# Performance work log

Measured on AMD Instinct MI355X. Metric: run time of the kernel, lower is better.

Reference implementation:

```python
import jax, jax.numpy as jnp
import numpy as np

CONV_LAYERS = [10, 10, 10]
DILATIONS = [1 << l for nl in CONV_LAYERS for l in range(nl)]  # 30 layers
B, C, S, V = 128, 64, 256, 256


def setup_inputs() -> dict:
    key = jax.random.key(0)
    ks = jax.random.split(key, 12)
    L = len(DILATIONS)
    sc = 0.1  # keep gated activations away from saturation
    return {
        "waveform_seed": jax.random.randint(ks[0], (B,), 0, V, dtype=jnp.int32),
        "embedding": jax.random.normal(ks[1], (V, C), jnp.float32) * sc,
        "kernels": jax.random.normal(ks[2], (L, 2, C, 2 * C), jnp.float32) * sc,
        "conv_bias": jax.random.normal(ks[3], (L, 2 * C), jnp.float32) * sc,
        "res_w": jax.random.normal(ks[4], (L, C, C), jnp.float32) * sc,
        "res_b": jax.random.normal(ks[5], (L, C), jnp.float32) * sc,
        "skip_w": jax.random.normal(ks[6], (L, C, S), jnp.float32) * sc,
        "skip_b": jax.random.normal(ks[7], (L, S), jnp.float32) * sc,
        "out_w0": jax.random.normal(ks[8], (S, V), jnp.float32) * sc,
        "out_b0": jax.random.normal(ks[9], (V,), jnp.float32) * sc,
        "out_w1": jax.random.normal(ks[10], (V, V), jnp.float32) * sc,
        "out_b1": jax.random.normal(ks[11], (V,), jnp.float32) * sc,
        "max_infer_samples": 128,
    }


def wavenet_generate(waveform_seed, embedding, kernels, conv_bias, res_w, res_b,
                     skip_w, skip_b, out_w0, out_b0, out_w1, out_b1, T):
    # Per-layer dilation queues (the tf queue_lst), initialized to zeros.
    bufs0 = tuple(jnp.zeros((d, B, C), embedding.dtype) for d in DILATIONS)

    def step(carry, _):
        bufs, idx = carry
        x = embedding[idx]                                   # (B, C) embedding lookup
        skip = jnp.zeros((B, S), x.dtype)
        new_bufs = []
        for i in range(len(DILATIONS)):
            buf = bufs[i]                                    # (d_i, B, C)
            x_last = buf[0]                                  # queue.pop(0)
            new_bufs.append(jnp.concatenate([buf[1:], x[None]], axis=0))  # queue.append(x_cur)
            # k=2 causal conv == two matmuls on (x_last, x_cur)
            h = x_last @ kernels[i, 0] + x @ kernels[i, 1] + conv_bias[i]  # (B, 2C)
            g = jnp.tanh(h[:, :C]) * jax.nn.sigmoid(h[:, C:])              # gated activation
            x = x + g @ res_w[i] + res_b[i]                   # residual out -> next layer input
            skip = skip + g @ skip_w[i] + skip_b[i]           # skip accumulation
        skip = jax.nn.relu(skip)
        h0 = jax.nn.relu(skip @ out_w0 + out_b0)
        logits = h0 @ out_w1 + out_b1                         # (B, V)
        nxt = jnp.argmax(logits, axis=-1).astype(jnp.int32)   # deterministic sampling
        return (tuple(new_bufs), nxt), (nxt, logits)

    _, (samples, logits) = jax.lax.scan(step, (bufs0, waveform_seed), None, length=T)
    # samples: (T, B) -> (B, T); logits: (T, B, V) -> (B, T, V)
    return samples.T, jnp.transpose(logits, (1, 0, 2))


def reference(waveform_seed, embedding, kernels, conv_bias, res_w, res_b,
              skip_w, skip_b, out_w0, out_b0, out_w1, out_b1, max_infer_samples):
    return wavenet_generate(waveform_seed, embedding, kernels, conv_bias, res_w, res_b,
                            skip_w, skip_b, out_w0, out_b0, out_w1, out_b1,
                            max_infer_samples)
```

## Files before the change

kernel.cpp:

```cpp
#include <hip/hip_runtime.h>
#include <hip/hip_bf16.h>
#include <math.h>


#define NL 30
#define NC 64
#define NS 256
#define NV 256
#define NB 128
#define QTOT 3069

__device__ float g_queues[(size_t)NB * QTOT * NC];

__global__ __launch_bounds__(256, 1)
void wavenet_gen_kernel(const int* __restrict__ seed,
                        const float* __restrict__ emb,
                        const float* __restrict__ kern,
                        const float* __restrict__ cbias,
                        const float* __restrict__ resw,
                        const float* __restrict__ resb,
                        const float* __restrict__ skipw,
                        const float* __restrict__ skipb,
                        const float* __restrict__ w0,
                        const float* __restrict__ b0,
                        const float* __restrict__ w1,
                        const float* __restrict__ b1,
                        const int* __restrict__ pT,
                        float* __restrict__ out)
{
  const int b = blockIdx.x;
  const int tid = threadIdx.x;
  const int T = pT[0];

  __shared__ float sx[NC];
  __shared__ float sxl[NC];
  __shared__ float shp[2][2 * NC];
  __shared__ float sg[NC];
  __shared__ float sskip[NS];
  __shared__ float sh0[NV];
  __shared__ float rv[4];
  __shared__ int   ri[4];
  __shared__ int   snext;

  if (tid < NC) sx[tid] = emb[(size_t)seed[b] * NC + tid];
  __syncthreads();

  float* __restrict__ q = g_queues + (size_t)b * QTOT * NC;
  const size_t logits_base = (size_t)NB * (size_t)T;

  for (int t = 0; t < T; ++t) {
    float skipacc = 0.f;
    int qoff = 0;

    for (int i = 0; i < NL; ++i) {
      const int d = 1 << (i % 10);

      if (tid < NC) {
        const int slot = t & (d - 1);
        float* qs = q + (size_t)(qoff + slot) * NC + tid;
        sxl[tid] = (t >= d) ? *qs : 0.f;
        *qs = sx[tid];
      }
      __syncthreads();

      {
        const int j = tid & 127;
        const int half = tid >> 7;
        const float* __restrict__ W =
            kern + ((size_t)(i * 2 + half)) * NC * 2 * NC + j;
        const float* __restrict__ xv = half ? sx : sxl;
        float acc = 0.f;
#pragma unroll
        for (int c = 0; c < NC; ++c) acc = fmaf(xv[c], W[(size_t)c * 2 * NC], acc);
        shp[half][j] = acc;
      }
      __syncthreads();

      if (tid < NC) {
        const float ha = shp[0][tid] + shp[1][tid] + cbias[i * 2 * NC + tid];
        const float hb = shp[0][tid + NC] + shp[1][tid + NC] + cbias[i * 2 * NC + NC + tid];
        sg[tid] = tanhf(ha) * (1.f / (1.f + expf(-hb)));
      }
      __syncthreads();

      {
        const float* __restrict__ SW = skipw + (size_t)i * NC * NS + tid;
        float acc = 0.f;
#pragma unroll
        for (int c = 0; c < NC; ++c) acc = fmaf(sg[c], SW[(size_t)c * NS], acc);
        skipacc += acc + skipb[i * NS + tid];
      }
      if (tid < NC) {
        const float* __restrict__ RW = resw + (size_t)i * NC * NC + tid;
        float acc = 0.f;
#pragma unroll
        for (int c = 0; c < NC; ++c) acc = fmaf(sg[c], RW[(size_t)c * NC], acc);
        sx[tid] = sx[tid] + acc + resb[i * NC + tid];
      }
      qoff += d;
      __syncthreads();
    }

    sskip[tid] = fmaxf(skipacc, 0.f);
    __syncthreads();
    {
      const float* __restrict__ W = w0 + tid;
      float acc = 0.f;
#pragma unroll 8
      for (int s = 0; s < NS; ++s) acc = fmaf(sskip[s], W[(size_t)s * NV], acc);
      sh0[tid] = fmaxf(acc + b0[tid], 0.f);
    }
    __syncthreads();
    float lg;
    {
      const float* __restrict__ W = w1 + tid;
      float acc = 0.f;
#pragma unroll 8
      for (int s = 0; s < NV; ++s) acc = fmaf(sh0[s], W[(size_t)s * NV], acc);
      lg = acc + b1[tid];
      out[logits_base + ((size_t)b * T + t) * NV + tid] = lg;
    }

    float v = lg;
    int ix = tid;
#pragma unroll
    for (int o = 32; o > 0; o >>= 1) {
      float ov = __shfl_down(v, o);
      int oi = __shfl_down(ix, o);
      if (ov > v || (ov == v && oi < ix)) { v = ov; ix = oi; }
    }
    if ((tid & 63) == 0) { rv[tid >> 6] = v; ri[tid >> 6] = ix; }
    __syncthreads();
    if (tid == 0) {
      float bv = rv[0];
      int bi = ri[0];
#pragma unroll
      for (int w = 1; w < 4; ++w)
        if (rv[w] > bv || (rv[w] == bv && ri[w] < bi)) { bv = rv[w]; bi = ri[w]; }
      snext = bi;
      out[(size_t)b * T + t] = (float)bi;
    }
    __syncthreads();

    if (tid < NC) sx[tid] = emb[(size_t)snext * NC + tid];
    __syncthreads();
  }
}

extern "C" void kernel_launch(void* const* d_in, const int* in_sizes, int n_in,
                              void* d_out, int out_size, void* d_ws, size_t ws_size,
                              hipStream_t stream) {
  (void)in_sizes; (void)n_in; (void)out_size; (void)d_ws; (void)ws_size;
  wavenet_gen_kernel<<<NB, 256, 0, stream>>>(
      (const int*)d_in[0],   (const float*)d_in[1], (const float*)d_in[2],
      (const float*)d_in[3], (const float*)d_in[4], (const float*)d_in[5],
      (const float*)d_in[6], (const float*)d_in[7], (const float*)d_in[8],
      (const float*)d_in[9], (const float*)d_in[10], (const float*)d_in[11],
      (const int*)d_in[12],  (float*)d_out);
}
```

Before: 14.15 ms.

## Split dot products across 4 threads and move queue traffic out of layer loop

Raises the block from 256 to 1024 threads, and splits every dot product over 4 lanes that are combined with xor shuffles, so each layer's serial FMA chain becomes a quarter as long. Per-layer queue reads and writes are taken off the critical path. Each layer's input is kept in a shared history buffer, and all 30 layers' delayed inputs are prefetched for the next step after the layer loop. This also removes one barrier per layer by merging the residual and skip phases. The cost is more threads per block, extra shuffle reductions and more shared memory.

```diff
diff --git a/kernel.cpp b/kernel.cpp
--- a/kernel.cpp
+++ b/kernel.cpp
@@ -9,10 +9,18 @@
 #define NV 256
 #define NB 128
 #define QTOT 3069
+#define NT 1024
 
 __device__ float g_queues[(size_t)NB * QTOT * NC];
 
-__global__ __launch_bounds__(256, 1)
+__device__ __forceinline__ void layer_params(int l, int& d, int& qo) {
+  const int a = (l >= 20) ? 2 : ((l >= 10) ? 1 : 0);
+  const int bb = l - a * 10;
+  d = 1 << bb;
+  qo = a * 1023 + (d - 1);
+}
+
+__global__ __launch_bounds__(NT, 1)
 void wavenet_gen_kernel(const int* __restrict__ seed,
                         const float* __restrict__ emb,
                         const float* __restrict__ kern,
@@ -28,21 +36,30 @@
                         const int* __restrict__ pT,
                         float* __restrict__ out)
 {
-  const int b = blockIdx.x;
-  const int tid = threadIdx.x;
-  const int T = pT[0];
-
-  __shared__ float sx[NC];
-  __shared__ float sxl[NC];
-  __shared__ float shp[2][2 * NC];
+  const int b   = blockIdx.x;
+  const int t_  = threadIdx.x;
+  const int T   = pT[0];
+
+  const int j    = t_ >> 2;
+  const int p    = t_ & 3;
+  const int half = j >> 7;
+  const int col  = j & 127;
+  const int lane = t_ & 63;
+  const int wv   = t_ >> 6;
+
+  __shared__ float sxlAll[NL][NC];
+  __shared__ float xHist[NL][NC];
+  __shared__ float hp[2][2 * NC];
   __shared__ float sg[NC];
   __shared__ float sskip[NS];
   __shared__ float sh0[NV];
-  __shared__ float rv[4];
-  __shared__ int   ri[4];
+  __shared__ float rv[16];
+  __shared__ int   ri[16];
   __shared__ int   snext;
 
-  if (tid < NC) sx[tid] = emb[(size_t)seed[b] * NC + tid];
+  ((float*)sxlAll)[t_] = 0.f;
+  if (t_ < (NL * NC - NT)) ((float*)sxlAll)[t_ + NT] = 0.f;
+  if (t_ < NC) xHist[0][t_] = emb[(size_t)seed[b] * NC + t_];
   __syncthreads();
 
   float* __restrict__ q = g_queues + (size_t)b * QTOT * NC;
@@ -50,99 +67,140 @@
 
   for (int t = 0; t < T; ++t) {
     float skipacc = 0.f;
-    int qoff = 0;
 
     for (int i = 0; i < NL; ++i) {
-      const int d = 1 << (i % 10);
-
-      if (tid < NC) {
-        const int slot = t & (d - 1);
-        float* qs = q + (size_t)(qoff + slot) * NC + tid;
-        sxl[tid] = (t >= d) ? *qs : 0.f;
-        *qs = sx[tid];
+      {
+        const float* __restrict__ W =
+            kern + ((size_t)(i * 2 + half)) * NC * (2 * NC) + col;
+        const float* __restrict__ xv = half ? xHist[i] : sxlAll[i];
+        float acc = 0.f;
+#pragma unroll
+        for (int cc = 0; cc < 16; ++cc) {
+          const int c = p * 16 + cc;
+          acc = fmaf(xv[c], W[(size_t)c * (2 * NC)], acc);
+        }
+        acc += __shfl_xor(acc, 1);
+        acc += __shfl_xor(acc, 2);
+        if (p == 0) hp[half][col] = acc;
       }
       __syncthreads();
 
+      if (t_ < NC) {
+        const float ha = hp[0][t_] + hp[1][t_] + cbias[i * 2 * NC + t_];
+        const float hb = hp[0][NC + t_] + hp[1][NC + t_] + cbias[i * 2 * NC + NC + t_];
+        sg[t_] = tanhf(ha) * (1.f / (1.f + expf(-hb)));
+      }
+      __syncthreads();
+
       {
-        const int j = tid & 127;
-        const int half = tid >> 7;
-        const float* __restrict__ W =
-            kern + ((size_t)(i * 2 + half)) * NC * 2 * NC + j;
-        const float* __restrict__ xv = half ? sx : sxl;
+        const float* __restrict__ SW = skipw + (size_t)i * NC * NS + j;
         float acc = 0.f;
 #pragma unroll
-        for (int c = 0; c < NC; ++c) acc = fmaf(xv[c], W[(size_t)c * 2 * NC], acc);
-        shp[half][j] = acc;
-      }
+        for (int cc = 0; cc < 16; ++cc) {
+          const int c = p * 16 + cc;
+          acc = fmaf(sg[c], SW[(size_t)c * NS], acc);
+        }
+        acc += __shfl_xor(acc, 1);
+        acc += __shfl_xor(acc, 2);
+        skipacc += acc + skipb[i * NS + j];
+      }
+      if (i < NL - 1 && t_ < 256) {
+        const float* __restrict__ RW = resw + (size_t)i * NC * NC + j;
+        float acc = 0.f;
+#pragma unroll
+        for (int cc = 0; cc < 16; ++cc) {
+          const int c = p * 16 + cc;
+          acc = fmaf(sg[c], RW[(size_t)c * NC], acc);
+        }
+        acc += __shfl_xor(acc, 1);
+        acc += __shfl_xor(acc, 2);
+        if (p == 0) xHist[i + 1][j] = xHist[i][j] + acc + resb[i * NC + j];
+      }
+      if (i == NL - 1 && p == 0) sskip[j] = fmaxf(skipacc, 0.f);
       __syncthreads();
-
-      if (tid < NC) {
-        const float ha = shp[0][tid] + shp[1][tid] + cbias[i * 2 * NC + tid];
-        const float hb = shp[0][tid + NC] + shp[1][tid + NC] + cbias[i * 2 * NC + NC + tid];
-        sg[tid] = tanhf(ha) * (1.f / (1.f + expf(-hb)));
-      }
-      __syncthreads();
-
-      {
-        const float* __restrict__ SW = skipw + (size_t)i * NC * NS + tid;
-        float acc = 0.f;
-#pragma unroll
-        for (int c = 0; c < NC; ++c) acc = fmaf(sg[c], SW[(size_t)c * NS], acc);
-        skipacc += acc + skipb[i * NS + tid];
-      }
-      if (tid < NC) {
-        const float* __restrict__ RW = resw + (size_t)i * NC * NC + tid;
-        float acc = 0.f;
-#pragma unroll
-        for (int c = 0; c < NC; ++c) acc = fmaf(sg[c], RW[(size_t)c * NC], acc);
-        sx[tid] = sx[tid] + acc + resb[i * NC + tid];
-      }
-      qoff += d;
-      __syncthreads();
-    }
-
-    sskip[tid] = fmaxf(skipacc, 0.f);
-    __syncthreads();
+    }
+
+    const int tp = t + 1;
+    float rA = 0.f, rB = 0.f;
     {
-      const float* __restrict__ W = w0 + tid;
-      float acc = 0.f;
-#pragma unroll 8
-      for (int s = 0; s < NS; ++s) acc = fmaf(sskip[s], W[(size_t)s * NV], acc);
-      sh0[tid] = fmaxf(acc + b0[tid], 0.f);
-    }
-    __syncthreads();
+      const int l0 = t_ >> 6;
+      int d0, qo0; layer_params(l0, d0, qo0);
+      if (d0 > 1 && tp >= d0)
+        rA = q[(size_t)(qo0 + (tp & (d0 - 1))) * NC + lane];
+      int l1 = l0 + 16, d1_ = 0, qo1 = 0;
+      const bool has1 = (t_ < (NL * NC - NT));
+      if (has1) {
+        layer_params(l1, d1_, qo1);
+        if (d1_ > 1 && tp >= d1_)
+          rB = q[(size_t)(qo1 + (tp & (d1_ - 1))) * NC + lane];
+      }
+      const float xv0 = xHist[l0][lane];
+      if (d0 == 1) rA = xv0;
+      else q[(size_t)(qo0 + (t & (d0 - 1))) * NC + lane] = xv0;
+      if (has1) {
+        const float xv1 = xHist[l1][lane];
+        if (d1_ == 1) rB = xv1;
+        else q[(size_t)(qo1 + (t & (d1_ - 1))) * NC + lane] = xv1;
+      }
+    }
+
+    {
+      const float* __restrict__ W = w0 + j;
+      float a0 = 0.f, a1 = 0.f;
+#pragma unroll
+      for (int cc = 0; cc < 64; cc += 2) {
+        const int c0 = 4 * cc + p;
+        const int c1 = 4 * (cc + 1) + p;
+        a0 = fmaf(sskip[c0], W[(size_t)c0 * NV], a0);
+        a1 = fmaf(sskip[c1], W[(size_t)c1 * NV], a1);
+      }
+      float acc = a0 + a1;
+      acc += __shfl_xor(acc, 1);
+      acc += __shfl_xor(acc, 2);
+      if (p == 0) sh0[j] = fmaxf(acc + b0[j], 0.f);
+    }
+    __syncthreads();
+
     float lg;
     {
-      const float* __restrict__ W = w1 + tid;
-      float acc = 0.f;
-#pragma unroll 8
-      for (int s = 0; s < NV; ++s) acc = fmaf(sh0[s], W[(size_t)s * NV], acc);
-      lg = acc + b1[tid];
-      out[logits_base + ((size_t)b * T + t) * NV + tid] = lg;
-    }
-
-    float v = lg;
-    int ix = tid;
+      const float* __restrict__ W = w1 + j;
+      float a0 = 0.f, a1 = 0.f;
+#pragma unroll
+      for (int cc = 0; cc < 64; cc += 2) {
+        const int c0 = 4 * cc + p;
+        const int c1 = 4 * (cc + 1) + p;
+        a0 = fmaf(sh0[c0], W[(size_t)c0 * NV], a0);
+        a1 = fmaf(sh0[c1], W[(size_t)c1 * NV], a1);
+      }
+      float acc = a0 + a1;
+      acc += __shfl_xor(acc, 1);
+      acc += __shfl_xor(acc, 2);
+      lg = acc + b1[j];
+      if (p == 0) out[logits_base + ((size_t)b * T + t) * NV + j] = lg;
+    }
+
+    float v = lg; int ix = j;
 #pragma unroll
     for (int o = 32; o > 0; o >>= 1) {
-      float ov = __shfl_down(v, o);
-      int oi = __shfl_down(ix, o);
+      const float ov = __shfl_down(v, o);
+      const int   oi = __shfl_down(ix, o);
       if (ov > v || (ov == v && oi < ix)) { v = ov; ix = oi; }
     }
-    if ((tid & 63) == 0) { rv[tid >> 6] = v; ri[tid >> 6] = ix; }
-    __syncthreads();
-    if (tid == 0) {
-      float bv = rv[0];
-      int bi = ri[0];
-#pragma unroll
-      for (int w = 1; w < 4; ++w)
+    if (lane == 0) { rv[wv] = v; ri[wv] = ix; }
+    __syncthreads();
+    if (t_ == 0) {
+      float bv = rv[0]; int bi = ri[0];
+#pragma unroll
+      for (int w = 1; w < 16; ++w)
         if (rv[w] > bv || (rv[w] == bv && ri[w] < bi)) { bv = rv[w]; bi = ri[w]; }
       snext = bi;
       out[(size_t)b * T + t] = (float)bi;
     }
     __syncthreads();
 
-    if (tid < NC) sx[tid] = emb[(size_t)snext * NC + tid];
+    ((float*)sxlAll)[t_] = rA;
+    if (t_ < (NL * NC - NT)) ((float*)sxlAll)[t_ + NT] = rB;
+    if (t_ < NC) xHist[0][t_] = emb[(size_t)snext * NC + t_];
     __syncthreads();
   }
 }
@@ -151,7 +209,7 @@
                               void* d_out, int out_size, void* d_ws, size_t ws_size,
                               hipStream_t stream) {
   (void)in_sizes; (void)n_in; (void)out_size; (void)d_ws; (void)ws_size;
-  wavenet_gen_kernel<<<NB, 256, 0, stream>>>(
+  wavenet_gen_kernel<<<NB, NT, 0, stream>>>(
       (const int*)d_in[0],   (const float*)d_in[1], (const float*)d_in[2],
       (const float*)d_in[3], (const float*)d_in[4], (const float*)d_in[5],
       (const float*)d_in[6], (const float*)d_in[7], (const float*)d_in[8],
```

New measurement: 54.63 ms. 3.86x slower.

## Restructure layer loop with dedicated queue warp, shuffled gates, fewer barriers

Applied to the files above, without the earlier changes.

Adds a fifth wavefront that handles the dilation queue writes and prefetches the queue reads two layers ahead into registers, so the serial global queue access leaves the critical path. The gate is computed redundantly in every wave and broadcast with shuffles, which drops the shared gate buffer and cuts the barriers per layer from four to two. Double-buffered x and xl arrays avoid read/write hazards, the tanh/sigmoid use fast exp intrinsics, and dot products use two accumulators. The costs are more threads per block, a more intricate prefetch schedule that can break causality if wrong, and slightly different gate rounding.

```diff
diff --git a/kernel.cpp b/kernel.cpp
--- a/kernel.cpp
+++ b/kernel.cpp
@@ -9,10 +9,24 @@
 #define NV 256
 #define NB 128
 #define QTOT 3069
+#define NT 320
 
 __device__ float g_queues[(size_t)NB * QTOT * NC];
 
-__global__ __launch_bounds__(256, 1)
+__device__ __forceinline__ void layer_params(int l, int& d, int& qo) {
+  const int a = (l >= 20) ? 2 : ((l >= 10) ? 1 : 0);
+  const int bb = l - a * 10;
+  d = 1 << bb;
+  qo = a * 1023 + (d - 1);
+}
+
+__device__ __forceinline__ float gate_fast(float ha, float hb) {
+  const float e2a = __expf(2.f * ha);
+  const float enb = __expf(-hb);
+  return (e2a - 1.f) / ((e2a + 1.f) * (1.f + enb));
+}
+
+__global__ __launch_bounds__(NT, 1)
 void wavenet_gen_kernel(const int* __restrict__ seed,
                         const float* __restrict__ emb,
                         const float* __restrict__ kern,
@@ -28,21 +42,27 @@
                         const int* __restrict__ pT,
                         float* __restrict__ out)
 {
-  const int b = blockIdx.x;
-  const int tid = threadIdx.x;
-  const int T = pT[0];
-
-  __shared__ float sx[NC];
-  __shared__ float sxl[NC];
-  __shared__ float shp[2][2 * NC];
-  __shared__ float sg[NC];
+  const int b    = blockIdx.x;
+  const int t_   = threadIdx.x;
+  const int T    = pT[0];
+  const int lane = t_ & 63;
+  const int w    = t_ >> 6;
+
+  __shared__ float xbuf[2][NC];
+  __shared__ float sxl[2][NC];
+  __shared__ float hp[2][2 * NC];
   __shared__ float sskip[NS];
   __shared__ float sh0[NV];
   __shared__ float rv[4];
   __shared__ int   ri[4];
   __shared__ int   snext;
 
-  if (tid < NC) sx[tid] = emb[(size_t)seed[b] * NC + tid];
+  if (t_ < NC) {
+    sxl[0][t_] = 0.f;
+    sxl[1][t_] = 0.f;
+    xbuf[0][t_] = emb[(size_t)seed[b] * NC + t_];
+  }
+  float rP0 = 0.f, rP1 = 0.f;
   __syncthreads();
 
   float* __restrict__ q = g_queues + (size_t)b * QTOT * NC;
@@ -50,99 +70,121 @@
 
   for (int t = 0; t < T; ++t) {
     float skipacc = 0.f;
-    int qoff = 0;
 
     for (int i = 0; i < NL; ++i) {
-      const int d = 1 << (i % 10);
-
-      if (tid < NC) {
-        const int slot = t & (d - 1);
-        float* qs = q + (size_t)(qoff + slot) * NC + tid;
-        sxl[tid] = (t >= d) ? *qs : 0.f;
-        *qs = sx[tid];
+      const int cb = i & 1;
+
+      if (w < 4) {
+        const int half = w & 1;
+        const int col  = ((w >> 1) << 6) + lane;
+        const float* __restrict__ W =
+            kern + ((size_t)(i * 2 + half)) * (NC * 2 * NC) + col;
+        const float* __restrict__ xv = half ? xbuf[cb] : sxl[cb];
+        float a0 = 0.f, a1 = 0.f;
+#pragma unroll
+        for (int c = 0; c < NC; c += 2) {
+          a0 = fmaf(xv[c],     W[(size_t)c * (2 * NC)],       a0);
+          a1 = fmaf(xv[c + 1], W[(size_t)(c + 1) * (2 * NC)], a1);
+        }
+        hp[half][col] = a0 + a1;
+      } else {
+        int d, qo; layer_params(i, d, qo);
+        q[(size_t)(qo + (t & (d - 1))) * NC + lane] = xbuf[cb][lane];
+        const int j = i + 2;
+        if (j < NL) {
+          int dj, qj; layer_params(j, dj, qj);
+          float v = 0.f;
+          if (t >= dj) v = q[(size_t)(qj + (t & (dj - 1))) * NC + lane];
+          if (cb) rP1 = v; else rP0 = v;
+        }
       }
       __syncthreads();
 
-      {
-        const int j = tid & 127;
-        const int half = tid >> 7;
-        const float* __restrict__ W =
-            kern + ((size_t)(i * 2 + half)) * NC * 2 * NC + j;
-        const float* __restrict__ xv = half ? sx : sxl;
-        float acc = 0.f;
-#pragma unroll
-        for (int c = 0; c < NC; ++c) acc = fmaf(xv[c], W[(size_t)c * 2 * NC], acc);
-        shp[half][j] = acc;
+      const float ha = hp[0][lane] + hp[1][lane] + cbias[i * 2 * NC + lane];
+      const float hb = hp[0][NC + lane] + hp[1][NC + lane]
+                     + cbias[i * 2 * NC + NC + lane];
+      const float sgv = gate_fast(ha, hb);
+
+      if (w < 4) {
+        const float* __restrict__ SW = skipw + (size_t)i * NC * NS + t_;
+        float a0 = 0.f, a1 = 0.f;
+#pragma unroll
+        for (int c = 0; c < NC; c += 2) {
+          a0 = fmaf(__shfl(sgv, c),     SW[(size_t)c * NS],       a0);
+          a1 = fmaf(__shfl(sgv, c + 1), SW[(size_t)(c + 1) * NS], a1);
+        }
+        skipacc += a0 + a1 + skipb[i * NS + t_];
+      } else {
+        if (i < NL - 1) {
+          const float* __restrict__ RW = resw + (size_t)i * NC * NC + lane;
+          float a0 = 0.f, a1 = 0.f;
+#pragma unroll
+          for (int c = 0; c < NC; c += 2) {
+            a0 = fmaf(__shfl(sgv, c),     RW[(size_t)c * NC],       a0);
+            a1 = fmaf(__shfl(sgv, c + 1), RW[(size_t)(c + 1) * NC], a1);
+          }
+          xbuf[cb ^ 1][lane] = xbuf[cb][lane] + a0 + a1 + resb[i * NC + lane];
+          sxl[cb ^ 1][lane] = (cb ^ 1) ? rP1 : rP0;
+        }
       }
       __syncthreads();
-
-      if (tid < NC) {
-        const float ha = shp[0][tid] + shp[1][tid] + cbias[i * 2 * NC + tid];
-        const float hb = shp[0][tid + NC] + shp[1][tid + NC] + cbias[i * 2 * NC + NC + tid];
-        sg[tid] = tanhf(ha) * (1.f / (1.f + expf(-hb)));
-      }
-      __syncthreads();
-
-      {
-        const float* __restrict__ SW = skipw + (size_t)i * NC * NS + tid;
-        float acc = 0.f;
-#pragma unroll
-        for (int c = 0; c < NC; ++c) acc = fmaf(sg[c], SW[(size_t)c * NS], acc);
-        skipacc += acc + skipb[i * NS + tid];
-      }
-      if (tid < NC) {
-        const float* __restrict__ RW = resw + (size_t)i * NC * NC + tid;
-        float acc = 0.f;
-#pragma unroll
-        for (int c = 0; c < NC; ++c) acc = fmaf(sg[c], RW[(size_t)c * NC], acc);
-        sx[tid] = sx[tid] + acc + resb[i * NC + tid];
-      }
-      qoff += d;
-      __syncthreads();
-    }
-
-    sskip[tid] = fmaxf(skipacc, 0.f);
-    __syncthreads();
-    {
-      const float* __restrict__ W = w0 + tid;
-      float acc = 0.f;
+    }
+
+    if (t_ < NS) {
+      sskip[t_] = fmaxf(skipacc, 0.f);
+    } else {
+      { int d, qo; layer_params(0, d, qo);
+        rP0 = (t + 1 >= d) ? q[(size_t)(qo + ((t + 1) & (d - 1))) * NC + lane] : 0.f; }
+      { int d, qo; layer_params(1, d, qo);
+        rP1 = (t + 1 >= d) ? q[(size_t)(qo + ((t + 1) & (d - 1))) * NC + lane] : 0.f; }
+    }
+    __syncthreads();
+
+    if (t_ < NV) {
+      const float* __restrict__ W = w0 + t_;
+      float a0 = 0.f, a1 = 0.f;
 #pragma unroll 8
-      for (int s = 0; s < NS; ++s) acc = fmaf(sskip[s], W[(size_t)s * NV], acc);
-      sh0[tid] = fmaxf(acc + b0[tid], 0.f);
-    }
-    __syncthreads();
-    float lg;
-    {
-      const float* __restrict__ W = w1 + tid;
-      float acc = 0.f;
+      for (int s = 0; s < NS; s += 2) {
+        a0 = fmaf(sskip[s],     W[(size_t)s * NV],       a0);
+        a1 = fmaf(sskip[s + 1], W[(size_t)(s + 1) * NV], a1);
+      }
+      sh0[t_] = fmaxf(a0 + a1 + b0[t_], 0.f);
+    }
+    __syncthreads();
+
+    if (t_ < NV) {
+      const float* __restrict__ W = w1 + t_;
+      float a0 = 0.f, a1 = 0.f;
 #pragma unroll 8
-      for (int s = 0; s < NV; ++s) acc = fmaf(sh0[s], W[(size_t)s * NV], acc);
-      lg = acc + b1[tid];
-      out[logits_base + ((size_t)b * T + t) * NV + tid] = lg;
-    }
-
-    float v = lg;
-    int ix = tid;
-#pragma unroll
-    for (int o = 32; o > 0; o >>= 1) {
-      float ov = __shfl_down(v, o);
-      int oi = __shfl_down(ix, o);
-      if (ov > v || (ov == v && oi < ix)) { v = ov; ix = oi; }
-    }
-    if ((tid & 63) == 0) { rv[tid >> 6] = v; ri[tid >> 6] = ix; }
-    __syncthreads();
-    if (tid == 0) {
-      float bv = rv[0];
-      int bi = ri[0];
-#pragma unroll
-      for (int w = 1; w < 4; ++w)
-        if (rv[w] > bv || (rv[w] == bv && ri[w] < bi)) { bv = rv[w]; bi = ri[w]; }
+      for (int s = 0; s < NV; s += 2) {
+        a0 = fmaf(sh0[s],     W[(size_t)s * NV],       a0);
+        a1 = fmaf(sh0[s + 1], W[(size_t)(s + 1) * NV], a1);
+      }
+      const float lg = a0 + a1 + b1[t_];
+      out[logits_base + ((size_t)b * T + t) * NV + t_] = lg;
+      float v = lg; int ix = t_;
+#pragma unroll
+      for (int o = 32; o > 0; o >>= 1) {
+        const float ov = __shfl_down(v, o);
+        const int   oi = __shfl_down(ix, o);
+        if (ov > v || (ov == v && oi < ix)) { v = ov; ix = oi; }
+      }
+      if (lane == 0) { rv[w] = v; ri[w] = ix; }
+    }
+    __syncthreads();
+
+    if (t_ == 0) {
+      float bv = rv[0]; int bi = ri[0];
+#pragma unroll
+      for (int k = 1; k < 4; ++k)
+        if (rv[k] > bv || (rv[k] == bv && ri[k] < bi)) { bv = rv[k]; bi = ri[k]; }
       snext = bi;
       out[(size_t)b * T + t] = (float)bi;
     }
-    __syncthreads();
-
-    if (tid < NC) sx[tid] = emb[(size_t)snext * NC + tid];
+    if (w == 4) sxl[0][lane] = rP0;
+    __syncthreads();
+
+    if (t_ < NC) xbuf[0][t_] = emb[(size_t)snext * NC + t_];
     __syncthreads();
   }
 }
@@ -151,7 +193,7 @@
                               void* d_out, int out_size, void* d_ws, size_t ws_size,
                               hipStream_t stream) {
   (void)in_sizes; (void)n_in; (void)out_size; (void)d_ws; (void)ws_size;
-  wavenet_gen_kernel<<<NB, 256, 0, stream>>>(
+  wavenet_gen_kernel<<<NB, NT, 0, stream>>>(
       (const int*)d_in[0],   (const float*)d_in[1], (const float*)d_in[2],
       (const float*)d_in[3], (const float*)d_in[4], (const float*)d_in[5],
       (const float*)d_in[6], (const float*)d_in[7], (const float*)d_in[8],
```

Result: faster. 12.57 ms (-11.2%).
